# Performance work log

Hardware: AMD Instinct MI355X
Metric: run time of the kernel (lower is better)

## Reference

```python
import jax, jax.numpy as jnp
import numpy as np

HEADS = 8
DIM_HEAD = 64
RMS_EPS = 1.1920929e-07  # torch default eps = finfo(fp32).eps


def rotate_half(x):
    x1, x2 = jnp.split(x, 2, axis=-1)
    return jnp.concatenate((-x2, x1), axis=-1)


def setup_inputs() -> dict:
    key = jax.random.key(0)
    k1, k2, k3, k4, k5 = jax.random.split(key, 5)
    b, n, dim = 2, 4096, 1024
    dim_hidden = HEADS * DIM_HEAD  # 512
    x = jax.random.normal(k1, (b, n, dim), dtype=jnp.float32)
    rotary_emb = jax.random.normal(k2, (n, DIM_HEAD), dtype=jnp.float32)
    rms_weight = jnp.ones((dim,), dtype=jnp.float32)
    w_qkv = jax.random.normal(k3, (dim, dim_hidden * 3), dtype=jnp.float32) * (dim ** -0.5)
    w_out = jax.random.normal(k4, (dim_hidden, dim), dtype=jnp.float32) * (dim_hidden ** -0.5)
    return {"x": x, "rotary_emb": rotary_emb, "rms_weight": rms_weight,
            "w_qkv": w_qkv, "w_out": w_out}


def reference(x, rotary_emb, rms_weight, w_qkv, w_out):
    b, n, dim = x.shape
    h, d = HEADS, DIM_HEAD
    # RMSNorm
    xn = x * jax.lax.rsqrt(jnp.mean(x * x, axis=-1, keepdims=True) + RMS_EPS) * rms_weight
    # QKV projection, rearrange 'b n (qkv h d) -> qkv b h n d'
    qkv = (xn @ w_qkv).reshape(b, n, 3, h, d).transpose(2, 0, 3, 1, 4)
    q, k, v = qkv[0], qkv[1], qkv[2]
    # RoPE
    cos, sin = jnp.cos(rotary_emb), jnp.sin(rotary_emb)  # (n, d) broadcasts over b,h
    q = q * cos + rotate_half(q) * sin
    k = k * cos + rotate_half(k) * sin
    q = q * (d ** -0.5)
    sim = jnp.einsum('bhid,bhjd->bhij', q, k)
    causal_mask = jnp.triu(jnp.ones((n, n), dtype=bool), 1)
    sim = jnp.where(causal_mask, -jnp.finfo(sim.dtype).max, sim)
    attn = jax.nn.softmax(sim, axis=-1)
    out = jnp.einsum('bhij,bhjd->bhid', attn, v)
    out = out.transpose(0, 2, 1, 3).reshape(b, n, h * d)  # 'b h n d -> b n (h d)'
    return out @ w_out
```

## Files before the change

kernel.cpp:

```cpp
#include <hip/hip_runtime.h>
#include <hip/hip_bf16.h>
#include <cstdint>

using bf16x8 = __attribute__((ext_vector_type(8))) __bf16;
using f32x4  = __attribute__((ext_vector_type(4))) float;

#define LOG2E 1.4426950408889634f

__device__ inline void gload16(__bf16* lds, const __bf16* g) {
    __builtin_amdgcn_global_load_lds((const __attribute__((address_space(1))) void*)g,
                                     (__attribute__((address_space(3))) void*)lds, 16, 0, 0);
}
__device__ inline void wait_barrier4() {
    asm volatile("s_waitcnt vmcnt(4)" ::: "memory");
    __builtin_amdgcn_s_barrier();
}
__device__ inline void wait_barrier0() {
    asm volatile("s_waitcnt vmcnt(0)" ::: "memory");
    __builtin_amdgcn_s_barrier();
}

__global__ __launch_bounds__(256) void rmsnorm_kernel(const float* __restrict__ x,
                                                      const float* __restrict__ w,
                                                      __bf16* __restrict__ xn) {
    const int row = blockIdx.x;
    const float4 v = reinterpret_cast<const float4*>(x + (size_t)row * 1024)[threadIdx.x];
    float ss = v.x * v.x + v.y * v.y + v.z * v.z + v.w * v.w;
#pragma unroll
    for (int i = 1; i < 64; i <<= 1) ss += __shfl_xor(ss, i);
    __shared__ float part[4];
    if ((threadIdx.x & 63) == 0) part[threadIdx.x >> 6] = ss;
    __syncthreads();
    const float total = part[0] + part[1] + part[2] + part[3];
    const float scale = rsqrtf(total * (1.0f / 1024.0f) + 1.1920929e-07f);
    const float4 wv = reinterpret_cast<const float4*>(w)[threadIdx.x];
    union { __bf16 h[4]; uint2 u; } pk;
    pk.h[0] = (__bf16)(v.x * scale * wv.x);
    pk.h[1] = (__bf16)(v.y * scale * wv.y);
    pk.h[2] = (__bf16)(v.z * scale * wv.z);
    pk.h[3] = (__bf16)(v.w * scale * wv.w);
    reinterpret_cast<uint2*>(xn + (size_t)row * 1024)[threadIdx.x] = pk.u;
}

__global__ void transpose_cast_kernel(const float* __restrict__ in,
                                      __bf16* __restrict__ out, int K, int N) {
    __shared__ float tile[32][33];
    const int n0 = blockIdx.x * 32, k0 = blockIdx.y * 32;
#pragma unroll
    for (int r = threadIdx.y; r < 32; r += 8)
        tile[r][threadIdx.x] = in[(size_t)(k0 + r) * N + n0 + threadIdx.x];
    __syncthreads();
#pragma unroll
    for (int r = threadIdx.y; r < 32; r += 8)
        out[(size_t)(n0 + r) * K + k0 + threadIdx.x] = (__bf16)tile[threadIdx.x][r];
}

__global__ __launch_bounds__(256) void csin_kernel(const float* __restrict__ rot,
                                                   float2* __restrict__ csin) {
    const int i = blockIdx.x * 256 + threadIdx.x;
    float s, c;
    sincosf(rot[i], &s, &c);
    csin[i] = make_float2(c, s);
}

__global__ __launch_bounds__(256) void rope_kernel(__bf16* __restrict__ qk,
                                                   const float2* __restrict__ csin) {
    const int row = blockIdx.x * 4 + (threadIdx.x >> 6);
    const int lane = threadIdx.x & 63;
    const int h = lane >> 3, dl = (lane & 7) * 4;
    const int pos = row & 4095;
    const float4 csA = *reinterpret_cast<const float4*>(&csin[pos * 64 + dl]);
    const float4 csB = *reinterpret_cast<const float4*>(&csin[pos * 64 + dl + 2]);
    const float4 csC = *reinterpret_cast<const float4*>(&csin[pos * 64 + dl + 32]);
    const float4 csD = *reinterpret_cast<const float4*>(&csin[pos * 64 + dl + 34]);
    const float c0[4] = {csA.x, csA.z, csB.x, csB.z};
    const float s0[4] = {csA.y, csA.w, csB.y, csB.w};
    const float c1[4] = {csC.x, csC.z, csD.x, csD.z};
    const float s1[4] = {csC.y, csC.w, csD.y, csD.w};
    __bf16* p = qk + (size_t)row * 1024 + h * 64 + dl;
    const float qs = 0.125f * LOG2E;
#pragma unroll
    for (int part = 0; part < 2; ++part) {
        __bf16* pp = p + part * 512;
        const float sc = part ? 1.0f : qs;
        union { uint2 u; __bf16 hh[4]; } va, vb, oa, ob;
        va.u = *reinterpret_cast<const uint2*>(pp);
        vb.u = *reinterpret_cast<const uint2*>(pp + 32);
#pragma unroll
        for (int j = 0; j < 4; ++j) {
            const float a = (float)va.hh[j], b2 = (float)vb.hh[j];
            oa.hh[j] = (__bf16)((a * c0[j] - b2 * s0[j]) * sc);
            ob.hh[j] = (__bf16)((b2 * c1[j] + a * s1[j]) * sc);
        }
        *reinterpret_cast<uint2*>(pp)      = oa.u;
        *reinterpret_cast<uint2*>(pp + 32) = ob.u;
    }
}

template <typename OutT, int MODE>
__global__ __launch_bounds__(256) void gemm_bt(const __bf16* __restrict__ A,
                                               const __bf16* __restrict__ Bt,
                                               OutT* __restrict__ C,
                                               __bf16* __restrict__ vt,
                                               int M, int N, int K) {
    __shared__ __align__(16) __bf16 As[3][128 * 32];
    __shared__ __align__(16) __bf16 Bs[3][128 * 32];
    const int bm = blockIdx.y, bn = blockIdx.x;
    const int tid = threadIdx.x;
    const int w = tid >> 6, l = tid & 63, lg = l >> 4, lr = l & 15;
    const int wr = w >> 1, wc = w & 1;
    const __bf16* Ab = A + (size_t)(bm * 128) * K;
    const __bf16* Bb = Bt + (size_t)(bn * 128) * K;
    const int srow = tid >> 2, scol = (tid & 3) * 8;
    const __bf16* Asrc = Ab + (size_t)srow * K + scol;
    const __bf16* Bsrc = Bb + (size_t)srow * K + scol;

    auto stage = [&](int k2) {
        const int nx = k2 % 3;
        const int off = k2 * 32;
        gload16(&As[nx][tid * 8],        Asrc + off);
        gload16(&As[nx][2048 + tid * 8], Asrc + (size_t)64 * K + off);
        gload16(&Bs[nx][tid * 8],        Bsrc + off);
        gload16(&Bs[nx][2048 + tid * 8], Bsrc + (size_t)64 * K + off);
    };

    const int NS = K >> 5;
    f32x4 acc[4][4] = {};
    stage(0);
    stage(1);
    wait_barrier4();
    for (int k = 0; k < NS; ++k) {
        const bool more = (k + 2 < NS);
        if (more) stage(k + 2);
        const __bf16* Ac = &As[k % 3][0];
        const __bf16* Bc = &Bs[k % 3][0];
        bf16x8 af[4], bfr[4];
#pragma unroll
        for (int m = 0; m < 4; ++m)
            af[m] = *reinterpret_cast<const bf16x8*>(Ac + (wr * 64 + m * 16 + lr) * 32 + lg * 8);
#pragma unroll
        for (int nn = 0; nn < 4; ++nn)
            bfr[nn] = *reinterpret_cast<const bf16x8*>(Bc + (wc * 64 + nn * 16 + lr) * 32 + lg * 8);
#pragma unroll
        for (int m = 0; m < 4; ++m)
#pragma unroll
            for (int nn = 0; nn < 4; ++nn)
                acc[m][nn] = __builtin_amdgcn_mfma_f32_16x16x32_bf16(af[m], bfr[nn],
                                                                     acc[m][nn], 0, 0, 0);
        if (more) wait_barrier4();
        else      wait_barrier0();
    }
    if constexpr (MODE == 1) {
        const int cb = bn * 128 + wc * 64;
        if (cb < 1024) {
#pragma unroll
            for (int m = 0; m < 4; ++m) {
                const int rg = bm * 128 + wr * 64 + m * 16 + 4 * lg;
#pragma unroll
                for (int nn = 0; nn < 4; ++nn) {
                    const int cg = cb + nn * 16 + lr;
#pragma unroll
                    for (int r = 0; r < 4; ++r)
                        C[(size_t)(rg + r) * 1024 + cg] = (OutT)acc[m][nn][r];
                }
            }
        } else {
#pragma unroll
            for (int m = 0; m < 4; ++m) {
                const int rg = bm * 128 + wr * 64 + m * 16 + 4 * lg;
                const int bidx = rg >> 12, pos0 = rg & 4095;
                const int a0 = pos0 & 63;
                const int cp = 32 * (a0 >> 5) + 8 * ((a0 >> 2) & 3) + 4 * ((a0 >> 4) & 1);
                const int nbase = (pos0 & ~63) + cp;
#pragma unroll
                for (int nn = 0; nn < 4; ++nn) {
                    const int col = cb + nn * 16 + lr - 1024;
                    const int hh = col >> 6, dd = col & 63;
                    union { __bf16 h4[4]; uint2 u; } pk2;
#pragma unroll
                    for (int r = 0; r < 4; ++r) pk2.h4[r] = (__bf16)acc[m][nn][r];
                    *reinterpret_cast<uint2*>(&vt[((size_t)(bidx * 8 + hh) * 64 + dd) * 4096 + nbase]) = pk2.u;
                }
            }
        }
        return;
    }
#pragma unroll
    for (int m = 0; m < 4; ++m) {
        const int rg = bm * 128 + wr * 64 + m * 16 + 4 * lg;
#pragma unroll
        for (int nn = 0; nn < 4; ++nn) {
            const int cg = bn * 128 + wc * 64 + nn * 16 + lr;
#pragma unroll
            for (int r = 0; r < 4; ++r)
                C[(size_t)(rg + r) * N + cg] = (OutT)acc[m][nn][r];
        }
    }
}

__global__ __launch_bounds__(256) void attn_kernel(const __bf16* __restrict__ qkp,
                                                   const __bf16* __restrict__ vt,
                                                   __bf16* __restrict__ attn_out) {
    const int bid = blockIdx.x;
    const int j = bid >> 3;
    const int bh = 2 * (bid & 7) + (j & 1);
    const int qt = 63 - (j >> 1);
    const int b = bh >> 3, h = bh & 7;
    const int tid = threadIdx.x;
    const int w = tid >> 6, l = tid & 63, lg = l >> 4, lr = l & 15;

    __shared__ __align__(16) __bf16 Ks[3][64 * 64];
    __shared__ __align__(16) __bf16 Vs[3][64 * 64];

    const __bf16* qbase = qkp + (size_t)b * 4096 * 1024 + h * 64;
    const __bf16* kbase = qbase + 512;
    const __bf16* vtb   = vt + (size_t)(b * 8 + h) * 64 * 4096;

    const int sr = tid >> 3;
    const int sc = ((tid & 7) ^ (sr & 7)) * 8;
    const __bf16* kp = kbase + (size_t)sr * 1024 + sc;
    const __bf16* vp = vtb + (size_t)sr * 4096 + sc;

    const int xel = (lr & 7) * 8;

    const int wq0 = qt * 64 + 16 * w;
    const int nkt = qt + 1;

    bf16x8 Qf[2];
#pragma unroll
    for (int kh = 0; kh < 2; ++kh)
        Qf[kh] = *reinterpret_cast<const bf16x8*>(
            qbase + (size_t)(wq0 + lr) * 1024 + 32 * kh + 8 * lg);

    bf16x8 ones;
#pragma unroll
    for (int i = 0; i < 8; ++i) ones[i] = (__bf16)1.0f;

    f32x4 O[4] = {};
    f32x4 Lacc = {};
    float m_ = -1e30f;

    auto stage2 = [&](__bf16* kdst, __bf16* vdst) {
        gload16(kdst + tid * 8,         kp);
        gload16(kdst + (tid + 256) * 8, kp + 32 * 1024);
        gload16(vdst + tid * 8,         vp);
        gload16(vdst + (tid + 256) * 8, vp + 32 * 4096);
        kp += 64 * 1024;
        vp += 64;
    };
    auto qk_step = [&](f32x4 (&S)[4], const __bf16* kb) {
        __builtin_amdgcn_s_setprio(1);
#pragma unroll
        for (int jt = 0; jt < 4; ++jt) {
            const __bf16* kr = kb + (16 * jt + lr) * 64;
            const bf16x8 Kf0 = *reinterpret_cast<const bf16x8*>(kr + ((8 * lg) ^ xel));
            const bf16x8 Kf1 = *reinterpret_cast<const bf16x8*>(kr + ((32 + 8 * lg) ^ xel));
            f32x4 z = {};
            z = __builtin_amdgcn_mfma_f32_16x16x32_bf16(Kf0, Qf[0], z, 0, 0, 0);
            S[jt] = __builtin_amdgcn_mfma_f32_16x16x32_bf16(Kf1, Qf[1], z, 0, 0, 0);
        }
        __builtin_amdgcn_s_setprio(0);
    };
    auto smpv = [&](f32x4 (&SC)[4], const __bf16* vb, bool domask) {
        if (domask) {
#pragma unroll
            for (int jt = 0; jt < 4; ++jt)
#pragma unroll
                for (int r = 0; r < 4; ++r)
                    if (16 * jt + 4 * lg + r > 16 * w + lr) SC[jt][r] = -1e30f;
        }
        float mx = -1e30f;
#pragma unroll
        for (int jt = 0; jt < 4; ++jt)
            mx = fmaxf(mx, fmaxf(fmaxf(SC[jt][0], SC[jt][1]), fmaxf(SC[jt][2], SC[jt][3])));
        if (__any(mx > m_ + 8.0f)) {
            mx = fmaxf(mx, __shfl_xor(mx, 16));
            mx = fmaxf(mx, __shfl_xor(mx, 32));
            const float mn = fmaxf(m_, mx);
            const float alpha = __builtin_amdgcn_exp2f(m_ - mn);
            m_ = mn;
            Lacc *= alpha;
#pragma unroll
            for (int dt = 0; dt < 4; ++dt) O[dt] *= alpha;
        }
#pragma unroll
        for (int jt = 0; jt < 4; ++jt)
#pragma unroll
            for (int r = 0; r < 4; ++r)
                SC[jt][r] = __builtin_amdgcn_exp2f(SC[jt][r] - m_);
        __builtin_amdgcn_s_setprio(1);
#pragma unroll
        for (int s = 0; s < 2; ++s) {
            bf16x8 Pf;
#pragma unroll
            for (int i = 0; i < 8; ++i)
                Pf[i] = (__bf16)SC[2 * s + (i >> 2)][i & 3];
            Lacc = __builtin_amdgcn_mfma_f32_16x16x32_bf16(ones, Pf, Lacc, 0, 0, 0);
#pragma unroll
            for (int dt = 0; dt < 4; ++dt) {
                const bf16x8 Vf = *reinterpret_cast<const bf16x8*>(
                    vb + (16 * dt + lr) * 64 + ((32 * s + 8 * lg) ^ xel));
                O[dt] = __builtin_amdgcn_mfma_f32_16x16x32_bf16(Vf, Pf, O[dt], 0, 0, 0);
            }
        }
        __builtin_amdgcn_s_setprio(0);
    };

    f32x4 S0[4], S1[4];
    int t = 0;

    stage2(Ks[0], Vs[0]);
    stage2(Ks[1], Vs[1]);
    __syncthreads();
    qk_step(S0, Ks[0]);

    for (; t + 8 <= nkt; t += 6) {
        stage2(Ks[2], Vs[2]); qk_step(S1, Ks[1]); smpv(S0, Vs[0], false); __syncthreads();
        stage2(Ks[0], Vs[0]); qk_step(S0, Ks[2]); smpv(S1, Vs[1], false); __syncthreads();
        stage2(Ks[1], Vs[1]); qk_step(S1, Ks[0]); smpv(S0, Vs[2], false); __syncthreads();
        stage2(Ks[2], Vs[2]); qk_step(S0, Ks[1]); smpv(S1, Vs[0], false); __syncthreads();
        stage2(Ks[0], Vs[0]); qk_step(S1, Ks[2]); smpv(S0, Vs[1], false); __syncthreads();
        stage2(Ks[1], Vs[1]); qk_step(S0, Ks[0]); smpv(S1, Vs[2], false); __syncthreads();
    }

    {
        f32x4 Sp[4];
#pragma unroll
        for (int jt = 0; jt < 4; ++jt) Sp[jt] = S0[jt];
        for (; t < nkt; ++t) {
            if (t + 2 < nkt) stage2(Ks[(t + 2) % 3], Vs[(t + 2) % 3]);
            f32x4 Sn[4];
            if (t + 1 < nkt) qk_step(Sn, Ks[(t + 1) % 3]);
            smpv(Sp, Vs[t % 3], t == nkt - 1);
            __syncthreads();
#pragma unroll
            for (int jt = 0; jt < 4; ++jt) Sp[jt] = Sn[jt];
        }
    }

    const float inv = 1.0f / Lacc[0];
    __bf16* op = attn_out + ((size_t)b * 4096 + wq0 + lr) * 512 + h * 64;
#pragma unroll
    for (int dt = 0; dt < 4; ++dt) {
        union { __bf16 h4[4]; uint2 u; } ow;
#pragma unroll
        for (int r = 0; r < 4; ++r) ow.h4[r] = (__bf16)(O[dt][r] * inv);
        *reinterpret_cast<uint2*>(op + 16 * dt + 4 * lg) = ow.u;
    }
}

extern "C" void kernel_launch(void* const* d_in, const int* in_sizes, int n_in,
                              void* d_out, int out_size, void* d_ws, size_t ws_size,
                              hipStream_t stream) {
    (void)in_sizes; (void)n_in; (void)out_size; (void)ws_size;
    const float* x    = (const float*)d_in[0];
    const float* rot  = (const float*)d_in[1];
    const float* rmsw = (const float*)d_in[2];
    const float* wqkv = (const float*)d_in[3];
    const float* wout = (const float*)d_in[4];
    float* out = (float*)d_out;

    char* ws = (char*)d_ws;
    __bf16* xn    = (__bf16*)ws;
    __bf16* wqkvt = (__bf16*)(ws + 16777216);
    __bf16* woutt = (__bf16*)(ws + 16777216 + 3145728);
    __bf16* aout  = (__bf16*)(ws + 16777216 + 3145728 + 1048576);
    __bf16* qk   = (__bf16*)d_out;
    float2* csin = (float2*)((char*)d_out + 16777216);
    __bf16* vt   = (__bf16*)((char*)d_out + 18874368);

    rmsnorm_kernel<<<8192, 256, 0, stream>>>(x, rmsw, xn);
    transpose_cast_kernel<<<dim3(48, 32), dim3(32, 8), 0, stream>>>(wqkv, wqkvt, 1024, 1536);
    transpose_cast_kernel<<<dim3(32, 16), dim3(32, 8), 0, stream>>>(wout, woutt, 512, 1024);
    csin_kernel<<<1024, 256, 0, stream>>>(rot, csin);
    gemm_bt<__bf16, 1><<<dim3(12, 64), 256, 0, stream>>>(xn, wqkvt, qk, vt, 8192, 1536, 1024);
    rope_kernel<<<2048, 256, 0, stream>>>(qk, csin);
    attn_kernel<<<1024, 256, 0, stream>>>(qk, vt, aout);
    gemm_bt<float, 0><<<dim3(8, 64), 256, 0, stream>>>(aout, woutt, out, nullptr, 8192, 1024, 512);
}
```

Before: 138.6 us.

## Fuse Q RoPE into attention, XCD-swizzle GEMM grids, double-buffer K

Q rotary embedding and softmax scaling now run inside the attention kernel when Q fragments are loaded, so the standalone RoPE pass handles only K and no longer reads and writes Q. The GEMM grids become 1D, and block indices are remapped so that consecutive row-blocks land on the same XCD, which should improve L2 reuse of the A tiles. The K shared-memory buffers drop from three to two, with an extra barrier added after the first QK step, to cut LDS use. The extra barrier and the reduced K buffering could introduce stalls.

```diff
diff --git a/kernel.cpp b/kernel.cpp
--- a/kernel.cpp
+++ b/kernel.cpp
@@ -63,8 +63,8 @@
     csin[i] = make_float2(c, s);
 }
 
-__global__ __launch_bounds__(256) void rope_kernel(__bf16* __restrict__ qk,
-                                                   const float2* __restrict__ csin) {
+__global__ __launch_bounds__(256) void rope_k_kernel(__bf16* __restrict__ qk,
+                                                     const float2* __restrict__ csin) {
     const int row = blockIdx.x * 4 + (threadIdx.x >> 6);
     const int lane = threadIdx.x & 63;
     const int h = lane >> 3, dl = (lane & 7) * 4;
@@ -77,24 +77,18 @@
     const float s0[4] = {csA.y, csA.w, csB.y, csB.w};
     const float c1[4] = {csC.x, csC.z, csD.x, csD.z};
     const float s1[4] = {csC.y, csC.w, csD.y, csD.w};
-    __bf16* p = qk + (size_t)row * 1024 + h * 64 + dl;
-    const float qs = 0.125f * LOG2E;
-#pragma unroll
-    for (int part = 0; part < 2; ++part) {
-        __bf16* pp = p + part * 512;
-        const float sc = part ? 1.0f : qs;
-        union { uint2 u; __bf16 hh[4]; } va, vb, oa, ob;
-        va.u = *reinterpret_cast<const uint2*>(pp);
-        vb.u = *reinterpret_cast<const uint2*>(pp + 32);
-#pragma unroll
-        for (int j = 0; j < 4; ++j) {
-            const float a = (float)va.hh[j], b2 = (float)vb.hh[j];
-            oa.hh[j] = (__bf16)((a * c0[j] - b2 * s0[j]) * sc);
-            ob.hh[j] = (__bf16)((b2 * c1[j] + a * s1[j]) * sc);
-        }
-        *reinterpret_cast<uint2*>(pp)      = oa.u;
-        *reinterpret_cast<uint2*>(pp + 32) = ob.u;
-    }
+    __bf16* pp = qk + (size_t)row * 1024 + 512 + h * 64 + dl;
+    union { uint2 u; __bf16 hh[4]; } va, vb, oa, ob;
+    va.u = *reinterpret_cast<const uint2*>(pp);
+    vb.u = *reinterpret_cast<const uint2*>(pp + 32);
+#pragma unroll
+    for (int j = 0; j < 4; ++j) {
+        const float a = (float)va.hh[j], b2 = (float)vb.hh[j];
+        oa.hh[j] = (__bf16)(a * c0[j] - b2 * s0[j]);
+        ob.hh[j] = (__bf16)(b2 * c1[j] + a * s1[j]);
+    }
+    *reinterpret_cast<uint2*>(pp)      = oa.u;
+    *reinterpret_cast<uint2*>(pp + 32) = ob.u;
 }
 
 template <typename OutT, int MODE>
@@ -105,7 +99,11 @@
                                                int M, int N, int K) {
     __shared__ __align__(16) __bf16 As[3][128 * 32];
     __shared__ __align__(16) __bf16 Bs[3][128 * 32];
-    const int bm = blockIdx.y, bn = blockIdx.x;
+    const int nbn = N >> 7;
+    const int xcd = blockIdx.x & 7;
+    const int idx = blockIdx.x >> 3;
+    const int bm = xcd * 8 + idx / nbn;
+    const int bn = idx % nbn;
     const int tid = threadIdx.x;
     const int w = tid >> 6, l = tid & 63, lg = l >> 4, lr = l & 15;
     const int wr = w >> 1, wc = w & 1;
@@ -200,6 +198,7 @@
 
 __global__ __launch_bounds__(256) void attn_kernel(const __bf16* __restrict__ qkp,
                                                    const __bf16* __restrict__ vt,
+                                                   const float2* __restrict__ csin,
                                                    __bf16* __restrict__ attn_out) {
     const int bid = blockIdx.x;
     const int j = bid >> 3;
@@ -209,7 +208,7 @@
     const int tid = threadIdx.x;
     const int w = tid >> 6, l = tid & 63, lg = l >> 4, lr = l & 15;
 
-    __shared__ __align__(16) __bf16 Ks[3][64 * 64];
+    __shared__ __align__(16) __bf16 Ks[2][64 * 64];
     __shared__ __align__(16) __bf16 Vs[3][64 * 64];
 
     const __bf16* qbase = qkp + (size_t)b * 4096 * 1024 + h * 64;
@@ -225,20 +224,6 @@
 
     const int wq0 = qt * 64 + 16 * w;
     const int nkt = qt + 1;
-
-    bf16x8 Qf[2];
-#pragma unroll
-    for (int kh = 0; kh < 2; ++kh)
-        Qf[kh] = *reinterpret_cast<const bf16x8*>(
-            qbase + (size_t)(wq0 + lr) * 1024 + 32 * kh + 8 * lg);
-
-    bf16x8 ones;
-#pragma unroll
-    for (int i = 0; i < 8; ++i) ones[i] = (__bf16)1.0f;
-
-    f32x4 O[4] = {};
-    f32x4 Lacc = {};
-    float m_ = -1e30f;
 
     auto stage2 = [&](__bf16* kdst, __bf16* vdst) {
         gload16(kdst + tid * 8,         kp);
@@ -248,6 +233,35 @@
         kp += 64 * 1024;
         vp += 64;
     };
+
+    stage2(Ks[0], Vs[0]);
+    stage2(Ks[1], Vs[1]);
+
+    bf16x8 Qf[2];
+    {
+        const __bf16* qp = qbase + (size_t)(wq0 + lr) * 1024 + 8 * lg;
+        const bf16x8 rq0 = *reinterpret_cast<const bf16x8*>(qp);
+        const bf16x8 rq1 = *reinterpret_cast<const bf16x8*>(qp + 32);
+        const float2* csp = csin + (size_t)(wq0 + lr) * 64 + 8 * lg;
+        const float qs = 0.125f * LOG2E;
+#pragma unroll
+        for (int i = 0; i < 8; ++i) {
+            const float2 ca = csp[i];
+            const float2 cb = csp[i + 32];
+            const float a = (float)rq0[i], b2 = (float)rq1[i];
+            Qf[0][i] = (__bf16)((a * ca.x - b2 * ca.y) * qs);
+            Qf[1][i] = (__bf16)((b2 * cb.x + a * cb.y) * qs);
+        }
+    }
+
+    bf16x8 ones;
+#pragma unroll
+    for (int i = 0; i < 8; ++i) ones[i] = (__bf16)1.0f;
+
+    f32x4 O[4] = {};
+    f32x4 Lacc = {};
+    float m_ = -1e30f;
+
     auto qk_step = [&](f32x4 (&S)[4], const __bf16* kb) {
         __builtin_amdgcn_s_setprio(1);
 #pragma unroll
@@ -309,17 +323,16 @@
     f32x4 S0[4], S1[4];
     int t = 0;
 
-    stage2(Ks[0], Vs[0]);
-    stage2(Ks[1], Vs[1]);
     __syncthreads();
     qk_step(S0, Ks[0]);
+    __syncthreads();
 
     for (; t + 8 <= nkt; t += 6) {
-        stage2(Ks[2], Vs[2]); qk_step(S1, Ks[1]); smpv(S0, Vs[0], false); __syncthreads();
-        stage2(Ks[0], Vs[0]); qk_step(S0, Ks[2]); smpv(S1, Vs[1], false); __syncthreads();
-        stage2(Ks[1], Vs[1]); qk_step(S1, Ks[0]); smpv(S0, Vs[2], false); __syncthreads();
-        stage2(Ks[2], Vs[2]); qk_step(S0, Ks[1]); smpv(S1, Vs[0], false); __syncthreads();
-        stage2(Ks[0], Vs[0]); qk_step(S1, Ks[2]); smpv(S0, Vs[1], false); __syncthreads();
+        stage2(Ks[0], Vs[2]); qk_step(S1, Ks[1]); smpv(S0, Vs[0], false); __syncthreads();
+        stage2(Ks[1], Vs[0]); qk_step(S0, Ks[0]); smpv(S1, Vs[1], false); __syncthreads();
+        stage2(Ks[0], Vs[1]); qk_step(S1, Ks[1]); smpv(S0, Vs[2], false); __syncthreads();
+        stage2(Ks[1], Vs[2]); qk_step(S0, Ks[0]); smpv(S1, Vs[0], false); __syncthreads();
+        stage2(Ks[0], Vs[0]); qk_step(S1, Ks[1]); smpv(S0, Vs[1], false); __syncthreads();
         stage2(Ks[1], Vs[1]); qk_step(S0, Ks[0]); smpv(S1, Vs[2], false); __syncthreads();
     }
 
@@ -328,9 +341,9 @@
 #pragma unroll
         for (int jt = 0; jt < 4; ++jt) Sp[jt] = S0[jt];
         for (; t < nkt; ++t) {
-            if (t + 2 < nkt) stage2(Ks[(t + 2) % 3], Vs[(t + 2) % 3]);
+            if (t + 2 < nkt) stage2(Ks[(t + 2) & 1], Vs[(t + 2) % 3]);
             f32x4 Sn[4];
-            if (t + 1 < nkt) qk_step(Sn, Ks[(t + 1) % 3]);
+            if (t + 1 < nkt) qk_step(Sn, Ks[(t + 1) & 1]);
             smpv(Sp, Vs[t % 3], t == nkt - 1);
             __syncthreads();
 #pragma unroll
@@ -373,8 +386,8 @@
     transpose_cast_kernel<<<dim3(48, 32), dim3(32, 8), 0, stream>>>(wqkv, wqkvt, 1024, 1536);
     transpose_cast_kernel<<<dim3(32, 16), dim3(32, 8), 0, stream>>>(wout, woutt, 512, 1024);
     csin_kernel<<<1024, 256, 0, stream>>>(rot, csin);
-    gemm_bt<__bf16, 1><<<dim3(12, 64), 256, 0, stream>>>(xn, wqkvt, qk, vt, 8192, 1536, 1024);
-    rope_kernel<<<2048, 256, 0, stream>>>(qk, csin);
-    attn_kernel<<<1024, 256, 0, stream>>>(qk, vt, aout);
-    gemm_bt<float, 0><<<dim3(8, 64), 256, 0, stream>>>(aout, woutt, out, nullptr, 8192, 1024, 512);
-}
+    gemm_bt<__bf16, 1><<<768, 256, 0, stream>>>(xn, wqkvt, qk, vt, 8192, 1536, 1024);
+    rope_k_kernel<<<2048, 256, 0, stream>>>(qk, csin);
+    attn_kernel<<<1024, 256, 0, stream>>>(qk, vt, csin, aout);
+    gemm_bt<float, 0><<<512, 256, 0, stream>>>(aout, woutt, out, nullptr, 8192, 1024, 512);
+}
```

After: 136.7 us. About the same (-1.4%).
